# Performance work log

Measured on AMD Instinct MI355X. Metric: run time of the kernel, lower is better.

The kernel has to match this reference:

```python
import jax, jax.numpy as jnp
import numpy as np

N_HEADS = 16

def setup_inputs() -> dict:
    key = jax.random.key(0)
    qkv = jax.random.normal(key, (4, 3072, 1024), dtype=jnp.float32)
    return {"qkv": qkv}

def reference(qkv):
    bs, width, length = qkv.shape
    ch = width // (3 * N_HEADS)
    qkv_h = qkv.reshape(bs * N_HEADS, 3 * ch, length)
    q, k, v = jnp.split(qkv_h, 3, axis=1)  # each [bs*H, ch, T]
    scale = 1.0 / jnp.sqrt(jnp.sqrt(jnp.asarray(ch, qkv.dtype)))
    # [bs*H, T, T] scores
    weight = jnp.einsum('bct,bcs->bts', q * scale, k * scale)
    weight = jax.nn.softmax(weight.astype(jnp.float32), axis=-1).astype(weight.dtype)
    a = jnp.einsum('bts,bcs->bct', weight, v)  # [bs*H, ch, T]
    return a.reshape(bs, -1, length)
```

## Files before the change

kernel.cpp:

```cpp
#include <hip/hip_runtime.h>
#include <hip/hip_bf16.h>


typedef __bf16 bf16_8 __attribute__((ext_vector_type(8)));
typedef __bf16 bf16_4 __attribute__((ext_vector_type(4)));
typedef float floatx4 __attribute__((ext_vector_type(4)));
typedef float floatx16 __attribute__((ext_vector_type(16)));

#define NTHREADS 512
#define STR 64
#define NSTEPS 16

#if __has_builtin(__builtin_amdgcn_exp2f)
#define EXP2(x) __builtin_amdgcn_exp2f(x)
#else
#define EXP2(x) exp2f(x)
#endif
#define QSCALE 0.18033688011112042f

#define LDS_BYTES 40960

#define ZERO16 (floatx16){0.f,0.f,0.f,0.f,0.f,0.f,0.f,0.f,0.f,0.f,0.f,0.f,0.f,0.f,0.f,0.f}

__device__ __forceinline__ int kap(int row) { return ((row >> 1) + (row >> 4)) & 7; }
__device__ __forceinline__ int sigma_row(int s) {
    return (s & 0x33) | ((s & 4) << 1) | ((s & 8) >> 1);
}

__device__ __forceinline__ unsigned pk_bf16(float a, float b) {
    unsigned r;
    asm("v_cvt_pk_bf16_f32 %0, %1, %2" : "=v"(r) : "v"(a), "v"(b));
    return r;
}

union U8 { unsigned u[4]; bf16_8 v; };
union U4 { unsigned u[2]; bf16_4 v; };

__device__ __forceinline__ void write_k(__bf16* kn, const float4* r, int si, int sG) {
    #pragma unroll
    for (int rr = 0; rr < 4; ++rr) {
        int srow = si * 4 + rr;
        int m = sigma_row(srow);
        U4 w;
        w.u[0] = pk_bf16(((const float*)&r[0])[rr], ((const float*)&r[1])[rr]);
        w.u[1] = pk_bf16(((const float*)&r[2])[rr], ((const float*)&r[3])[rr]);
        *(bf16_4*)&kn[m * STR + ((sG ^ (kap(m) << 1)) << 2)] = w.v;
    }
}
__device__ __forceinline__ void write_v(__bf16* vn, const float4* r, int si, int c0) {
    #pragma unroll
    for (int jj = 0; jj < 4; ++jj) {
        int c = c0 + jj;
        U4 w;
        w.u[0] = pk_bf16(r[jj].x, r[jj].y);
        w.u[1] = pk_bf16(r[jj].z, r[jj].w);
        *(bf16_4*)&vn[c * STR + ((si ^ (kap(c) << 1)) << 2)] = w.v;
    }
}

__global__ __launch_bounds__(NTHREADS, 4)
void attn_kernel(const float* __restrict__ qkv, float* __restrict__ out) {
    __shared__ char smem[LDS_BYTES];
    __bf16* k0  = (__bf16*)smem;
    __bf16* k1  = (__bf16*)(smem + 8192);
    __bf16* v0  = (__bf16*)(smem + 16384);
    __bf16* v1  = (__bf16*)(smem + 24576);
    __bf16* v2  = (__bf16*)(smem + 32768);

    const int tid  = threadIdx.x;
    const int wave = tid >> 6;
    const int lane = tid & 63;
    const int hv   = lane >> 5;
    const int l31  = lane & 31;
    const int g    = wave >> 1;
    const int sh   = wave & 1;

    const int bx = blockIdx.x;
    const int bh = bx & 63;
    const int t0 = (bx >> 6) << 7;

    const float* qg = qkv + (size_t)bh * 196608;
    const float* kg = qg + 65536;
    const float* vg = qg + 131072;

    const int sv = tid >> 8;
    const int st = tid & 255;
    const int si = st & 15;
    const int sG = st >> 4;
    const int c0 = sG << 2;
    const float* gsrc = sv ? vg : kg;

    float4 r4[4];
    #pragma unroll
    for (int jj = 0; jj < 4; ++jj)
        r4[jj] = *(const float4*)(gsrc + (c0 + jj) * 1024 + si * 4);

    bf16_8 qf[4];
    {
        const int tq = t0 + g * 32 + l31;
        #pragma unroll
        for (int kc = 0; kc < 4; ++kc) {
            U8 w;
            #pragma unroll
            for (int d = 0; d < 4; ++d) {
                float f0 = qg[(16 * kc + 8 * hv + 2 * d) * 1024 + tq] * QSCALE;
                float f1 = qg[(16 * kc + 8 * hv + 2 * d + 1) * 1024 + tq] * QSCALE;
                w.u[d] = pk_bf16(f0, f1);
            }
            qf[kc] = w.v;
        }
    }

    float4 prA[4];
    #pragma unroll
    for (int jj = 0; jj < 4; ++jj)
        prA[jj] = *(const float4*)(gsrc + (c0 + jj) * 1024 + 64 + si * 4);

    if (!sv) write_k(k0, r4, si, sG);
    else     write_v(v0, r4, si, c0);
    __syncthreads();

    floatx16 O0 = ZERO16, O1 = ZERO16;
    float l = 0.f;
    bf16_8 pfp0, pfp1;
    int vprev = 2, vcur = 0, vnext = 1;

    const int krow = sh * 32 + l31;
    const int kx   = kap(krow);
    const int vx0  = kap(l31);
    const int vx1  = kap(32 + l31);

    for (int is = 0; is < NSTEPS; ++is) {
        const __bf16* kb = (is & 1) ? k1 : k0;

        float4 prB[4];
        if (is < NSTEPS - 2) {
            const int s0n = (is + 2) * 64;
            #pragma unroll
            for (int jj = 0; jj < 4; ++jj)
                prB[jj] = *(const float4*)(gsrc + (c0 + jj) * 1024 + s0n + si * 4);
        }

        floatx16 St = ZERO16;
        __builtin_amdgcn_s_setprio(1);
        #pragma unroll
        for (int kc = 0; kc < 4; ++kc) {
            bf16_8 kf = *(const bf16_8*)&kb[krow * STR + ((((kc << 1) | hv) ^ kx) << 3)];
            St = __builtin_amdgcn_mfma_f32_32x32x16_bf16(kf, qf[kc], St, 0, 0, 0);
        }
        __builtin_amdgcn_s_setprio(0);

        U8 w0, w1;
        #pragma unroll
        for (int d = 0; d < 4; ++d) {
            float pa = EXP2(St[2 * d]);
            float pb = EXP2(St[2 * d + 1]);
            float pc = EXP2(St[8 + 2 * d]);
            float pd = EXP2(St[8 + 2 * d + 1]);
            l += (pa + pb) + (pc + pd);
            w0.u[d] = pk_bf16(pa, pb);
            w1.u[d] = pk_bf16(pc, pd);
        }
        bf16_8 pfn0 = w0.v, pfn1 = w1.v;

        if (is > 0) {
            const __bf16* vp = (vprev == 0) ? v0 : ((vprev == 1) ? v1 : v2);
            __builtin_amdgcn_s_setprio(1);
            {
                int vrow = l31;
                bf16_8 vfa = *(const bf16_8*)&vp[vrow * STR + ((((sh << 2) | hv) ^ vx0) << 3)];
                O0 = __builtin_amdgcn_mfma_f32_32x32x16_bf16(vfa, pfp0, O0, 0, 0, 0);
                bf16_8 vfb = *(const bf16_8*)&vp[vrow * STR + ((((sh << 2) | 2 | hv) ^ vx0) << 3)];
                O0 = __builtin_amdgcn_mfma_f32_32x32x16_bf16(vfb, pfp1, O0, 0, 0, 0);
            }
            {
                int vrow = 32 + l31;
                bf16_8 vfa = *(const bf16_8*)&vp[vrow * STR + ((((sh << 2) | hv) ^ vx1) << 3)];
                O1 = __builtin_amdgcn_mfma_f32_32x32x16_bf16(vfa, pfp0, O1, 0, 0, 0);
                bf16_8 vfb = *(const bf16_8*)&vp[vrow * STR + ((((sh << 2) | 2 | hv) ^ vx1) << 3)];
                O1 = __builtin_amdgcn_mfma_f32_32x32x16_bf16(vfb, pfp1, O1, 0, 0, 0);
            }
            __builtin_amdgcn_s_setprio(0);
        }
        pfp0 = pfn0; pfp1 = pfn1;

        if (is < NSTEPS - 1) {
            if (!sv) {
                __bf16* kn = (is & 1) ? k0 : k1;
                write_k(kn, prA, si, sG);
            } else {
                __bf16* vn = (vnext == 0) ? v0 : ((vnext == 1) ? v1 : v2);
                write_v(vn, prA, si, c0);
            }
            __syncthreads();
        }
        #pragma unroll
        for (int jj = 0; jj < 4; ++jj) prA[jj] = prB[jj];
        vprev = vcur; vcur = vnext; vnext = (vnext == 2) ? 0 : vnext + 1;
    }

    {
        const __bf16* vp = (vprev == 0) ? v0 : ((vprev == 1) ? v1 : v2);
        {
            int vrow = l31;
            bf16_8 vfa = *(const bf16_8*)&vp[vrow * STR + ((((sh << 2) | hv) ^ vx0) << 3)];
            O0 = __builtin_amdgcn_mfma_f32_32x32x16_bf16(vfa, pfp0, O0, 0, 0, 0);
            bf16_8 vfb = *(const bf16_8*)&vp[vrow * STR + ((((sh << 2) | 2 | hv) ^ vx0) << 3)];
            O0 = __builtin_amdgcn_mfma_f32_32x32x16_bf16(vfb, pfp1, O0, 0, 0, 0);
        }
        {
            int vrow = 32 + l31;
            bf16_8 vfa = *(const bf16_8*)&vp[vrow * STR + ((((sh << 2) | hv) ^ vx1) << 3)];
            O1 = __builtin_amdgcn_mfma_f32_32x32x16_bf16(vfa, pfp0, O1, 0, 0, 0);
            bf16_8 vfb = *(const bf16_8*)&vp[vrow * STR + ((((sh << 2) | 2 | hv) ^ vx1) << 3)];
            O1 = __builtin_amdgcn_mfma_f32_32x32x16_bf16(vfb, pfp1, O1, 0, 0, 0);
        }
    }

    l += __shfl_xor(l, 32);

    __syncthreads();
    float* xo = (float*)smem;
    float* xl = (float*)(smem + 32768);
    if (sh == 1) {
        float* b = xo + g * 2048;
        #pragma unroll
        for (int rq = 0; rq < 4; ++rq) {
            floatx4 a0 = {O0[4 * rq], O0[4 * rq + 1], O0[4 * rq + 2], O0[4 * rq + 3]};
            *(floatx4*)&b[(rq * 64 + lane) * 4] = a0;
            floatx4 a1 = {O1[4 * rq], O1[4 * rq + 1], O1[4 * rq + 2], O1[4 * rq + 3]};
            *(floatx4*)&b[((4 + rq) * 64 + lane) * 4] = a1;
        }
        xl[g * 64 + lane] = l;
    }
    __syncthreads();
    if (sh == 0) {
        const float* b = xo + g * 2048;
        const float lt = l + xl[g * 64 + lane];
        const float linv = 1.0f / lt;
        float* og = out + (size_t)bh * 65536 + t0 + g * 32;
        #pragma unroll
        for (int rq = 0; rq < 4; ++rq) {
            floatx4 a0 = *(const floatx4*)&b[(rq * 64 + lane) * 4];
            floatx4 a1 = *(const floatx4*)&b[((4 + rq) * 64 + lane) * 4];
            #pragma unroll
            for (int j = 0; j < 4; ++j) {
                int cl = j + 8 * rq + 4 * hv;
                og[cl * 1024 + l31] = (O0[4 * rq + j] + a0[j]) * linv;
                og[(32 + cl) * 1024 + l31] = (O1[4 * rq + j] + a1[j]) * linv;
            }
        }
    }
}

extern "C" void kernel_launch(void* const* d_in, const int* in_sizes, int n_in,
                              void* d_out, int out_size, void* d_ws, size_t ws_size,
                              hipStream_t stream) {
    const float* qkv = (const float*)d_in[0];
    float* out = (float*)d_out;
    attn_kernel<<<dim3(512), dim3(NTHREADS), 0, stream>>>(qkv, out);
}
```

Measured before the change: 126.1 us.

## Process key/value tiles in pairs with double-buffered LDS and half the barriers

The main loop now handles two 64-key tiles per iteration, ping-ponging between two LDS buffers that each hold a K and V tile pair. This replaces the triple-buffered V ring with its one-step-delayed PV MFMA and the per-tile __syncthreads. Global prefetch of the next pair is issued at the start of each iteration, and the LDS writes are interleaved between compute phases, so there is one barrier per pair instead of one per tile. The cost is more LDS (64 KB vs 40 KB) and more live registers for two prefetched tiles, which could lower occupancy; the s_setprio hints are also dropped.

```diff
diff --git a/kernel.cpp b/kernel.cpp
--- a/kernel.cpp
+++ b/kernel.cpp
@@ -9,7 +9,7 @@
 
 #define NTHREADS 512
 #define STR 64
-#define NSTEPS 16
+#define NPAIRS 8
 
 #if __has_builtin(__builtin_amdgcn_exp2f)
 #define EXP2(x) __builtin_amdgcn_exp2f(x)
@@ -18,9 +18,15 @@
 #endif
 #define QSCALE 0.18033688011112042f
 
-#define LDS_BYTES 40960
+#define LDS_BYTES 65536
 
 #define ZERO16 (floatx16){0.f,0.f,0.f,0.f,0.f,0.f,0.f,0.f,0.f,0.f,0.f,0.f,0.f,0.f,0.f,0.f}
+
+#define BAR() do {                                          \
+    asm volatile("s_waitcnt lgkmcnt(0)" ::: "memory");      \
+    __builtin_amdgcn_s_barrier();                           \
+    __builtin_amdgcn_sched_barrier(0);                      \
+} while (0)
 
 __device__ __forceinline__ int kap(int row) { return ((row >> 1) + (row >> 4)) & 7; }
 __device__ __forceinline__ int sigma_row(int s) {
@@ -61,11 +67,10 @@
 __global__ __launch_bounds__(NTHREADS, 4)
 void attn_kernel(const float* __restrict__ qkv, float* __restrict__ out) {
     __shared__ char smem[LDS_BYTES];
-    __bf16* k0  = (__bf16*)smem;
-    __bf16* k1  = (__bf16*)(smem + 8192);
-    __bf16* v0  = (__bf16*)(smem + 16384);
-    __bf16* v1  = (__bf16*)(smem + 24576);
-    __bf16* v2  = (__bf16*)(smem + 32768);
+    __bf16* kp0 = (__bf16*)smem;
+    __bf16* kp1 = (__bf16*)(smem + 16384);
+    __bf16* vp0 = (__bf16*)(smem + 32768);
+    __bf16* vp1 = (__bf16*)(smem + 49152);
 
     const int tid  = threadIdx.x;
     const int wave = tid >> 6;
@@ -90,11 +95,6 @@
     const int c0 = sG << 2;
     const float* gsrc = sv ? vg : kg;
 
-    float4 r4[4];
-    #pragma unroll
-    for (int jj = 0; jj < 4; ++jj)
-        r4[jj] = *(const float4*)(gsrc + (c0 + jj) * 1024 + si * 4);
-
     bf16_8 qf[4];
     {
         const int tq = t0 + g * 32 + l31;
@@ -111,46 +111,51 @@
         }
     }
 
-    float4 prA[4];
-    #pragma unroll
-    for (int jj = 0; jj < 4; ++jj)
-        prA[jj] = *(const float4*)(gsrc + (c0 + jj) * 1024 + 64 + si * 4);
-
-    if (!sv) write_k(k0, r4, si, sG);
-    else     write_v(v0, r4, si, c0);
+    {
+        #pragma unroll
+        for (int t = 0; t < 2; ++t) {
+            float4 r4[4];
+            #pragma unroll
+            for (int jj = 0; jj < 4; ++jj)
+                r4[jj] = *(const float4*)(gsrc + (c0 + jj) * 1024 + t * 64 + si * 4);
+            if (!sv) write_k(kp0 + t * 4096, r4, si, sG);
+            else     write_v(vp0 + t * 4096, r4, si, c0);
+        }
+    }
     __syncthreads();
 
     floatx16 O0 = ZERO16, O1 = ZERO16;
     float l = 0.f;
-    bf16_8 pfp0, pfp1;
-    int vprev = 2, vcur = 0, vnext = 1;
 
     const int krow = sh * 32 + l31;
     const int kx   = kap(krow);
     const int vx0  = kap(l31);
     const int vx1  = kap(32 + l31);
 
-    for (int is = 0; is < NSTEPS; ++is) {
-        const __bf16* kb = (is & 1) ? k1 : k0;
-
-        float4 prB[4];
-        if (is < NSTEPS - 2) {
-            const int s0n = (is + 2) * 64;
+    for (int p = 0; p < NPAIRS; ++p) {
+        const __bf16* kb = (p & 1) ? kp1 : kp0;
+        const __bf16* vb = (p & 1) ? vp1 : vp0;
+        __bf16* kn = (p & 1) ? kp0 : kp1;
+        __bf16* vn = (p & 1) ? vp0 : vp1;
+
+        float4 rA[4], rB[4];
+        if (p < NPAIRS - 1) {
+            const int s0n = (2 * p + 2) * 64;
             #pragma unroll
             for (int jj = 0; jj < 4; ++jj)
-                prB[jj] = *(const float4*)(gsrc + (c0 + jj) * 1024 + s0n + si * 4);
+                rA[jj] = *(const float4*)(gsrc + (c0 + jj) * 1024 + s0n + si * 4);
+            #pragma unroll
+            for (int jj = 0; jj < 4; ++jj)
+                rB[jj] = *(const float4*)(gsrc + (c0 + jj) * 1024 + s0n + 64 + si * 4);
         }
 
         floatx16 St = ZERO16;
-        __builtin_amdgcn_s_setprio(1);
         #pragma unroll
         for (int kc = 0; kc < 4; ++kc) {
             bf16_8 kf = *(const bf16_8*)&kb[krow * STR + ((((kc << 1) | hv) ^ kx) << 3)];
             St = __builtin_amdgcn_mfma_f32_32x32x16_bf16(kf, qf[kc], St, 0, 0, 0);
         }
-        __builtin_amdgcn_s_setprio(0);
-
-        U8 w0, w1;
+        U8 wa0, wa1;
         #pragma unroll
         for (int d = 0; d < 4; ++d) {
             float pa = EXP2(St[2 * d]);
@@ -158,63 +163,76 @@
             float pc = EXP2(St[8 + 2 * d]);
             float pd = EXP2(St[8 + 2 * d + 1]);
             l += (pa + pb) + (pc + pd);
-            w0.u[d] = pk_bf16(pa, pb);
-            w1.u[d] = pk_bf16(pc, pd);
-        }
-        bf16_8 pfn0 = w0.v, pfn1 = w1.v;
-
-        if (is > 0) {
-            const __bf16* vp = (vprev == 0) ? v0 : ((vprev == 1) ? v1 : v2);
-            __builtin_amdgcn_s_setprio(1);
+            wa0.u[d] = pk_bf16(pa, pb);
+            wa1.u[d] = pk_bf16(pc, pd);
+        }
+        bf16_8 pfa0 = wa0.v, pfa1 = wa1.v;
+
+        if (p < NPAIRS - 1) {
+            if (!sv) write_k(kn, rA, si, sG);
+            else     write_v(vn, rA, si, c0);
+        }
+
+        floatx16 Su = ZERO16;
+        #pragma unroll
+        for (int kc = 0; kc < 4; ++kc) {
+            bf16_8 kf = *(const bf16_8*)&kb[4096 + krow * STR + ((((kc << 1) | hv) ^ kx) << 3)];
+            Su = __builtin_amdgcn_mfma_f32_32x32x16_bf16(kf, qf[kc], Su, 0, 0, 0);
+        }
+        U8 wb0, wb1;
+        #pragma unroll
+        for (int d = 0; d < 4; ++d) {
+            float pa = EXP2(Su[2 * d]);
+            float pb = EXP2(Su[2 * d + 1]);
+            float pc = EXP2(Su[8 + 2 * d]);
+            float pd = EXP2(Su[8 + 2 * d + 1]);
+            l += (pa + pb) + (pc + pd);
+            wb0.u[d] = pk_bf16(pa, pb);
+            wb1.u[d] = pk_bf16(pc, pd);
+        }
+        bf16_8 pfb0 = wb0.v, pfb1 = wb1.v;
+        {
+            const __bf16* vp = vb;
             {
                 int vrow = l31;
                 bf16_8 vfa = *(const bf16_8*)&vp[vrow * STR + ((((sh << 2) | hv) ^ vx0) << 3)];
-                O0 = __builtin_amdgcn_mfma_f32_32x32x16_bf16(vfa, pfp0, O0, 0, 0, 0);
+                O0 = __builtin_amdgcn_mfma_f32_32x32x16_bf16(vfa, pfa0, O0, 0, 0, 0);
                 bf16_8 vfb = *(const bf16_8*)&vp[vrow * STR + ((((sh << 2) | 2 | hv) ^ vx0) << 3)];
-                O0 = __builtin_amdgcn_mfma_f32_32x32x16_bf16(vfb, pfp1, O0, 0, 0, 0);
+                O0 = __builtin_amdgcn_mfma_f32_32x32x16_bf16(vfb, pfa1, O0, 0, 0, 0);
             }
             {
                 int vrow = 32 + l31;
                 bf16_8 vfa = *(const bf16_8*)&vp[vrow * STR + ((((sh << 2) | hv) ^ vx1) << 3)];
-                O1 = __builtin_amdgcn_mfma_f32_32x32x16_bf16(vfa, pfp0, O1, 0, 0, 0);
+                O1 = __builtin_amdgcn_mfma_f32_32x32x16_bf16(vfa, pfa0, O1, 0, 0, 0);
                 bf16_8 vfb = *(const bf16_8*)&vp[vrow * STR + ((((sh << 2) | 2 | hv) ^ vx1) << 3)];
-                O1 = __builtin_amdgcn_mfma_f32_32x32x16_bf16(vfb, pfp1, O1, 0, 0, 0);
-            }
-            __builtin_amdgcn_s_setprio(0);
-        }
-        pfp0 = pfn0; pfp1 = pfn1;
-
-        if (is < NSTEPS - 1) {
-            if (!sv) {
-                __bf16* kn = (is & 1) ? k0 : k1;
-                write_k(kn, prA, si, sG);
-            } else {
-                __bf16* vn = (vnext == 0) ? v0 : ((vnext == 1) ? v1 : v2);
-                write_v(vn, prA, si, c0);
-            }
-            __syncthreads();
-        }
-        #pragma unroll
-        for (int jj = 0; jj < 4; ++jj) prA[jj] = prB[jj];
-        vprev = vcur; vcur = vnext; vnext = (vnext == 2) ? 0 : vnext + 1;
-    }
-
-    {
-        const __bf16* vp = (vprev == 0) ? v0 : ((vprev == 1) ? v1 : v2);
+                O1 = __builtin_amdgcn_mfma_f32_32x32x16_bf16(vfb, pfa1, O1, 0, 0, 0);
+            }
+        }
+
+        if (p < NPAIRS - 1) {
+            if (!sv) write_k(kn + 4096, rB, si, sG);
+            else     write_v(vn + 4096, rB, si, c0);
+        }
+
         {
-            int vrow = l31;
-            bf16_8 vfa = *(const bf16_8*)&vp[vrow * STR + ((((sh << 2) | hv) ^ vx0) << 3)];
-            O0 = __builtin_amdgcn_mfma_f32_32x32x16_bf16(vfa, pfp0, O0, 0, 0, 0);
-            bf16_8 vfb = *(const bf16_8*)&vp[vrow * STR + ((((sh << 2) | 2 | hv) ^ vx0) << 3)];
-            O0 = __builtin_amdgcn_mfma_f32_32x32x16_bf16(vfb, pfp1, O0, 0, 0, 0);
-        }
-        {
-            int vrow = 32 + l31;
-            bf16_8 vfa = *(const bf16_8*)&vp[vrow * STR + ((((sh << 2) | hv) ^ vx1) << 3)];
-            O1 = __builtin_amdgcn_mfma_f32_32x32x16_bf16(vfa, pfp0, O1, 0, 0, 0);
-            bf16_8 vfb = *(const bf16_8*)&vp[vrow * STR + ((((sh << 2) | 2 | hv) ^ vx1) << 3)];
-            O1 = __builtin_amdgcn_mfma_f32_32x32x16_bf16(vfb, pfp1, O1, 0, 0, 0);
-        }
+            const __bf16* vp = vb + 4096;
+            {
+                int vrow = l31;
+                bf16_8 vfa = *(const bf16_8*)&vp[vrow * STR + ((((sh << 2) | hv) ^ vx0) << 3)];
+                O0 = __builtin_amdgcn_mfma_f32_32x32x16_bf16(vfa, pfb0, O0, 0, 0, 0);
+                bf16_8 vfb = *(const bf16_8*)&vp[vrow * STR + ((((sh << 2) | 2 | hv) ^ vx0) << 3)];
+                O0 = __builtin_amdgcn_mfma_f32_32x32x16_bf16(vfb, pfb1, O0, 0, 0, 0);
+            }
+            {
+                int vrow = 32 + l31;
+                bf16_8 vfa = *(const bf16_8*)&vp[vrow * STR + ((((sh << 2) | hv) ^ vx1) << 3)];
+                O1 = __builtin_amdgcn_mfma_f32_32x32x16_bf16(vfa, pfb0, O1, 0, 0, 0);
+                bf16_8 vfb = *(const bf16_8*)&vp[vrow * STR + ((((sh << 2) | 2 | hv) ^ vx1) << 3)];
+                O1 = __builtin_amdgcn_mfma_f32_32x32x16_bf16(vfb, pfb1, O1, 0, 0, 0);
+            }
+        }
+
+        if (p < NPAIRS - 1) BAR();
     }
 
     l += __shfl_xor(l, 32);
```

Measured after the change: 132.2 us. 4.8% more time.
